# Optimization experiments

Measured on AMD Instinct MI355X. Metric: run time of the kernel, lower is better.

## Reference

```python
import jax, jax.numpy as jnp
import numpy as np

DIM = 768
NUM_HEADS = 12
HEAD_DIM = DIM // NUM_HEADS
SCALE = HEAD_DIM ** -0.5


def setup_inputs() -> dict:
    key = jax.random.key(0)
    ks = jax.random.split(key, 5)
    b, n = 8, 1024
    x = jax.random.normal(ks[0], (b, n, DIM), dtype=jnp.float32)
    # qkv Linear weight: torch stores (out, in) = (3*DIM, DIM)
    w_qkv = jax.random.normal(ks[1], (3 * DIM, DIM), dtype=jnp.float32) * (DIM ** -0.5)
    q_bias = jax.random.normal(ks[2], (DIM,), dtype=jnp.float32) * 0.02
    v_bias = jax.random.normal(ks[3], (DIM,), dtype=jnp.float32) * 0.02
    w_proj = jax.random.normal(ks[4], (DIM, DIM), dtype=jnp.float32) * (DIM ** -0.5)
    b_proj = jnp.zeros((DIM,), dtype=jnp.float32)
    return {"x": x, "w_qkv": w_qkv, "q_bias": q_bias, "v_bias": v_bias,
            "w_proj": w_proj, "b_proj": b_proj}


def reference(x, w_qkv, q_bias, v_bias, w_proj, b_proj):
    b, n, _ = x.shape
    # qkv bias: [q_bias, zeros, v_bias]
    qkv_bias = jnp.concatenate([q_bias, jnp.zeros_like(v_bias), v_bias])
    qkv = x @ w_qkv.T + qkv_bias                      # (b, n, 3*DIM)
    qkv = qkv.reshape(b, n, 3, NUM_HEADS, HEAD_DIM)
    qkv = jnp.transpose(qkv, (2, 0, 3, 1, 4))          # (3, b, h, n, d)
    q, k, v = qkv[0], qkv[1], qkv[2]
    q = q * SCALE
    attn = jnp.einsum('bhqd,bhkd->bhqk', q, k)         # (b, h, n, n)
    attn = jax.nn.softmax(attn, axis=-1)
    out = jnp.einsum('bhqk,bhkd->bhqd', attn, v)       # (b, h, n, d)
    out = jnp.transpose(out, (0, 2, 1, 3)).reshape(b, n, NUM_HEADS * HEAD_DIM)
    return out @ w_proj.T + b_proj
```

## Files before the change

### kernel.cpp

```cpp
#include <hip/hip_runtime.h>
#include <math.h>

#define BATCH 8
#define SEQ   1024
#define DIM   768
#define NH    12
#define HD    64
#define MROWS 8192
#define NQKV  2304
#define KDIM  768
#define QSCALE 0.18033688011112042f

typedef unsigned short u16;
typedef unsigned int   u32;
typedef __attribute__((ext_vector_type(8))) short bf16x8;
typedef __attribute__((ext_vector_type(4))) float f32x4;
typedef __attribute__((ext_vector_type(16))) float f32x16;

__device__ __forceinline__ u16 f2bf(float f){
  u32 u = __builtin_bit_cast(u32, f);
  u += 0x7FFFu + ((u >> 16) & 1u);
  return (u16)(u >> 16);
}

__device__ __forceinline__ void gload16(const void* g, void* l){
  __builtin_amdgcn_global_load_lds((const __attribute__((address_space(1))) u32*)g,
                                   (__attribute__((address_space(3))) u32*)l, 16, 0, 0);
}

__device__ __forceinline__ f32x16 zero16(){
  return (f32x16){0.f,0.f,0.f,0.f,0.f,0.f,0.f,0.f,0.f,0.f,0.f,0.f,0.f,0.f,0.f,0.f};
}

__global__ __launch_bounds__(256) void convert_bf16(
    const float* __restrict__ x, const float* __restrict__ wq,
    const float* __restrict__ wp, u16* __restrict__ xb,
    u16* __restrict__ wqb, u16* __restrict__ wpb){
  const long n1 = (long)MROWS*DIM/8, n2 = (long)NQKV*DIM/8, n3 = (long)DIM*DIM/8;
  long i = (long)blockIdx.x*blockDim.x + threadIdx.x;
  const float* s; u16* d;
  if (i < n1)            { s = x  + i*8;        d = xb  + i*8; }
  else if (i < n1+n2)    { long j=i-n1;    s = wq + j*8; d = wqb + j*8; }
  else if (i < n1+n2+n3) { long j=i-n1-n2; s = wp + j*8; d = wpb + j*8; }
  else return;
  float4 a = ((const float4*)s)[0];
  float4 b = ((const float4*)s)[1];
  union { u16 h[8]; uint4 v; } o;
  o.h[0]=f2bf(a.x); o.h[1]=f2bf(a.y); o.h[2]=f2bf(a.z); o.h[3]=f2bf(a.w);
  o.h[4]=f2bf(b.x); o.h[5]=f2bf(b.y); o.h[6]=f2bf(b.z); o.h[7]=f2bf(b.w);
  *((uint4*)d) = o.v;
}

__global__ __launch_bounds__(512, 4) void qkv_gemm(
    const u16* __restrict__ xb, const u16* __restrict__ wb,
    const float* __restrict__ qbias, const float* __restrict__ vbias,
    u16* __restrict__ qo, u16* __restrict__ ko, u16* __restrict__ vto){
  __shared__ u16 As[16384];
  __shared__ u16 Bs[16384];
  const int tid = threadIdx.x;
  const int wid = tid >> 6, lane = tid & 63;
  const int lr = lane & 15, lg = lane >> 4;
  const int wm = wid >> 2, wn = wid & 3;
  const int swz = (blockIdx.x & 7) * 144 + (blockIdx.x >> 3);
  const int bm = swz / 18, bn = swz % 18;
  const int mbase = bm * 128, nbase = bn * 128;
  const int sr8 = tid >> 3;
  const int sc8 = ((tid & 7) ^ (sr8 & 7)) * 8;
  const u16* aS = xb + (size_t)(mbase + sr8) * KDIM + sc8;
  const u16* bS = wb + (size_t)(nbase + sr8) * KDIM + sc8;
  u16* aD = As + tid * 8;
  u16* bD = Bs + tid * 8;

#define STAGEQ(buf, k0) do {                                                  \
    gload16(aS + (k0),            aD + (buf)*8192);                           \
    gload16(aS + (k0) + 64*KDIM,  aD + (buf)*8192 + 4096);                    \
    gload16(bS + (k0),            bD + (buf)*8192);                           \
    gload16(bS + (k0) + 64*KDIM,  bD + (buf)*8192 + 4096);                    \
  } while(0)

  f32x4 acc[4][2];
  #pragma unroll
  for (int a=0;a<4;++a)
    #pragma unroll
    for (int b=0;b<2;++b) acc[a][b] = (f32x4){0.f,0.f,0.f,0.f};

  STAGEQ(0, 0);
  __syncthreads();

  for (int kt = 0; kt < 12; ++kt){
    const int cur = kt & 1;
    if (kt < 11) STAGEQ(cur ^ 1, (kt+1)*64);
    const u16* Ac = As + cur*8192;
    const u16* Bc = Bs + cur*8192;
    bf16x8 af[2][4], bfv[2][2];
    #pragma unroll
    for (int kk = 0; kk < 2; ++kk){
      const int ch = (((kk*4 + lg)) ^ (lr & 7)) * 8;
      #pragma unroll
      for (int f = 0; f < 4; ++f)
        af[kk][f]  = *(const bf16x8*)(Ac + (wm*64 + f*16 + lr)*64 + ch);
      #pragma unroll
      for (int g = 0; g < 2; ++g)
        bfv[kk][g] = *(const bf16x8*)(Bc + (wn*32 + g*16 + lr)*64 + ch);
    }
    #pragma unroll
    for (int fm = 0; fm < 4; ++fm)
      #pragma unroll
      for (int fn = 0; fn < 2; ++fn){
        acc[fm][fn] = __builtin_amdgcn_mfma_f32_16x16x32_bf16(af[0][fm], bfv[0][fn], acc[fm][fn], 0,0,0);
        acc[fm][fn] = __builtin_amdgcn_mfma_f32_16x16x32_bf16(af[1][fm], bfv[1][fn], acc[fm][fn], 0,0,0);
      }
    __syncthreads();
  }
#undef STAGEQ

  const int which = bn / 6;
  const int bb = mbase >> 10, nn0 = mbase & 1023;
  if (which == 2){
    const int vcol0 = nbase - 1536;
    float bv[2];
    #pragma unroll
    for (int fn = 0; fn < 2; ++fn) bv[fn] = vbias[vcol0 + wn*32 + fn*16 + lr];
    u16* Ls = As;
    #pragma unroll
    for (int h = 0; h < 2; ++h){
      __syncthreads();
      if (wm == h){
        #pragma unroll
        for (int fn = 0; fn < 2; ++fn){
          const int n = wn*32 + fn*16 + lr;
          #pragma unroll
          for (int fm = 0; fm < 4; ++fm)
            #pragma unroll
            for (int r = 0; r < 4; ++r){
              const int mloc = fm*16 + lg*4 + r;
              Ls[n*64 + (((mloc>>3) ^ (n&7))*8) + (mloc&7)] = f2bf(acc[fm][fn][r] + bv[fn]);
            }
        }
      }
      __syncthreads();
      const int n = tid >> 2, q4 = tid & 3;
      const int col = vcol0 + n;
      u16* drow = vto + ((size_t)((bb*NH + (col>>6))*HD + (col&63)))*SEQ + nn0 + h*64;
      #pragma unroll
      for (int j2 = 0; j2 < 2; ++j2){
        const int j = q4*2 + j2;
        *(uint4*)(drow + j*8) = *(const uint4*)(Ls + n*64 + ((j ^ (n&7))*8));
      }
    }
  } else {
    const int mrow0 = mbase + wm*64;
    const int ncol0 = nbase - which*768 + wn*32;
    #pragma unroll
    for (int fn = 0; fn < 2; ++fn){
      const int col = ncol0 + fn*16 + lr;
      const int hh = col >> 6, dd = col & 63;
      const float bias = (which == 0) ? qbias[col] : 0.f;
      #pragma unroll
      for (int fm = 0; fm < 4; ++fm){
        #pragma unroll
        for (int r = 0; r < 4; ++r){
          const int m = mrow0 + fm*16 + lg*4 + r;
          const int head = (m >> 10)*NH + hh;
          const float v = acc[fm][fn][r] + bias;
          if (which == 0) qo[((size_t)head*SEQ + (m & 1023))*HD + dd] = f2bf(v * QSCALE);
          else            ko[((size_t)head*SEQ + (m & 1023))*HD + dd] = f2bf(v);
        }
      }
    }
  }
}

__global__ __launch_bounds__(256, 3) void attn_kernel(
    const u16* __restrict__ qg, const u16* __restrict__ kg,
    const u16* __restrict__ vtg, u16* __restrict__ og){
  __shared__ u16 Ks[3*4096];
  __shared__ u16 VTs[3*4096];
  const int tid  = threadIdx.x;
  const int wid  = tid >> 6, lane = tid & 63;
  const int l31  = lane & 31, hi = lane >> 5, l7 = lane & 7;
  const int bid  = blockIdx.x;
  const int swz  = (bid & 7) * 96 + (bid >> 3);
  const int head = swz >> 3;
  const int qbase = (swz & 7) * 128;
  const u16* Q  = qg  + (size_t)head * SEQ * HD;
  const u16* K  = kg  + (size_t)head * SEQ * HD;
  const u16* VT = vtg + (size_t)head * HD * SEQ;

  const int qrow = qbase + wid*32 + l31;
  bf16x8 qf[4];
  #pragma unroll
  for (int dc = 0; dc < 4; ++dc)
    qf[dc] = *(const bf16x8*)(Q + (size_t)qrow*HD + dc*16 + hi*8);

  f32x16 oacc[2];
  oacc[0] = zero16(); oacc[1] = zero16();
  float lrow = 0.f;

  bf16x8 vfr[8];
  bf16x8 pa[4];

  const int srow   = lane >> 3;
  const int schunk = ((lane & 7) ^ srow) * 8;

#define STAGE(bufi, kv0) do {                                                 \
    const u16* ksrc = K + (size_t)((kv0) + wid*16 + srow)*HD + schunk;        \
    gload16(ksrc,         &Ks[(bufi)*4096 + wid*1024]);                       \
    gload16(ksrc + 8*HD,  &Ks[(bufi)*4096 + wid*1024 + 512]);                 \
    const u16* vsrc = VT + (size_t)(wid*16 + srow)*SEQ + (kv0) + schunk;      \
    gload16(vsrc,         &VTs[(bufi)*4096 + wid*1024]);                      \
    gload16(vsrc + 8*SEQ, &VTs[(bufi)*4096 + wid*1024 + 512]);                \
  } while(0)

  STAGE(0, 0);
  STAGE(1, 64);

  #pragma unroll
  for (int t = 0; t < 16; ++t){
    const int cur = t % 3;
    if (t < 15) asm volatile("s_waitcnt vmcnt(4) lgkmcnt(0)" ::: "memory");
    else        asm volatile("s_waitcnt vmcnt(0) lgkmcnt(0)" ::: "memory");
    __builtin_amdgcn_s_barrier();
    if (t < 14) STAGE((t+2)%3, (t+2)*64);

    const u16* Kc  = &Ks[cur*4096];
    const u16* VTc = &VTs[cur*4096];

    f32x16 sv[2];
    __builtin_amdgcn_s_setprio(1);
    #pragma unroll
    for (int b = 0; b < 2; ++b){
      sv[b] = zero16();
      #pragma unroll
      for (int dc = 0; dc < 4; ++dc){
        bf16x8 kf = *(const bf16x8*)(&Kc[(b*32 + l31)*64 + (((dc*2 + hi) ^ l7) * 8)]);
        sv[b] = __builtin_amdgcn_mfma_f32_32x32x16_bf16(kf, qf[dc], sv[b], 0,0,0);
      }
    }
    if (t > 0){
      #pragma unroll
      for (int kc = 0; kc < 4; ++kc)
        #pragma unroll
        for (int db = 0; db < 2; ++db)
          oacc[db] = __builtin_amdgcn_mfma_f32_32x32x16_bf16(pa[kc], vfr[kc*2+db], oacc[db], 0,0,0);
    }
    __builtin_amdgcn_s_setprio(0);

    #pragma unroll
    for (int kc = 0; kc < 4; ++kc)
      #pragma unroll
      for (int db = 0; db < 2; ++db)
        vfr[kc*2+db] = *(const bf16x8*)(&VTc[(db*32 + l31)*64 + (((kc*2 + hi) ^ l7) * 8)]);

    float tsum[16];
    #pragma unroll
    for (int i = 0; i < 16; ++i){
      float p0 = __builtin_amdgcn_exp2f(sv[0][i]);
      float p1 = __builtin_amdgcn_exp2f(sv[1][i]);
      sv[0][i] = p0; sv[1][i] = p1;
      tsum[i] = p0 + p1;
    }
    #pragma unroll
    for (int st = 8; st > 0; st >>= 1)
      #pragma unroll
      for (int i = 0; i < st; ++i) tsum[i] += tsum[i + st];
    const float ssum = tsum[0];
    lrow += ssum + __shfl_xor(ssum, 32);

    #pragma unroll
    for (int b = 0; b < 2; ++b){
      u32 x0,x1,x2,x3,y0,y1,y2,y3;
      asm("v_cvt_pk_bf16_f32 %0, %1, %2" : "=v"(x0) : "v"(sv[b][0]),  "v"(sv[b][1]));
      asm("v_cvt_pk_bf16_f32 %0, %1, %2" : "=v"(y0) : "v"(sv[b][4]),  "v"(sv[b][5]));
      asm("v_cvt_pk_bf16_f32 %0, %1, %2" : "=v"(x1) : "v"(sv[b][2]),  "v"(sv[b][3]));
      asm("v_cvt_pk_bf16_f32 %0, %1, %2" : "=v"(y1) : "v"(sv[b][6]),  "v"(sv[b][7]));
      asm("v_permlane32_swap_b32 %0, %1" : "+v"(x0), "+v"(y0));
      asm("v_permlane32_swap_b32 %0, %1" : "+v"(x1), "+v"(y1));
      asm("v_cvt_pk_bf16_f32 %0, %1, %2" : "=v"(x2) : "v"(sv[b][8]),  "v"(sv[b][9]));
      asm("v_cvt_pk_bf16_f32 %0, %1, %2" : "=v"(y2) : "v"(sv[b][12]), "v"(sv[b][13]));
      asm("v_cvt_pk_bf16_f32 %0, %1, %2" : "=v"(x3) : "v"(sv[b][10]), "v"(sv[b][11]));
      asm("v_cvt_pk_bf16_f32 %0, %1, %2" : "=v"(y3) : "v"(sv[b][14]), "v"(sv[b][15]));
      asm("v_permlane32_swap_b32 %0, %1" : "+v"(x2), "+v"(y2));
      asm("v_permlane32_swap_b32 %0, %1" : "+v"(x3), "+v"(y3));
      union { u32 w[4]; bf16x8 f; } fa, fb;
      fa.w[0]=x0; fa.w[1]=x1; fa.w[2]=y0; fa.w[3]=y1;
      fb.w[0]=x2; fb.w[1]=x3; fb.w[2]=y2; fb.w[3]=y3;
      pa[b*2]   = fa.f;
      pa[b*2+1] = fb.f;
    }
  }
#undef STAGE

  __builtin_amdgcn_s_setprio(1);
  #pragma unroll
  for (int kc = 0; kc < 4; ++kc)
    #pragma unroll
    for (int db = 0; db < 2; ++db)
      oacc[db] = __builtin_amdgcn_mfma_f32_32x32x16_bf16(pa[kc], vfr[kc*2+db], oacc[db], 0,0,0);
  __builtin_amdgcn_s_setprio(0);

  const float inv = 1.f / lrow;
  const int bb = head / NH, hh = head % NH;
  #pragma unroll
  for (int r = 0; r < 16; ++r){
    const int q = (r&3) + 8*(r>>2) + 4*hi;
    const float s = __shfl(inv, q);
    const int n = qbase + wid*32 + q;
    u16* orow = og + (size_t)(bb*SEQ + n)*DIM + hh*HD;
    orow[l31]      = f2bf(oacc[0][r] * s);
    orow[32 + l31] = f2bf(oacc[1][r] * s);
  }
}

__global__ __launch_bounds__(256) void proj_gemm(
    const u16* __restrict__ ab, const u16* __restrict__ wb,
    const float* __restrict__ bias, float* __restrict__ out){
  __shared__ u16 As2[2*4096];
  __shared__ u16 Bs2[2*8192];
  const int tid = threadIdx.x;
  const int wid = tid >> 6, lane = tid & 63;
  const int lr = lane & 15, lg = lane >> 4;
  const int wm = wid >> 1, wn = wid & 1;
  const int swz = (blockIdx.x & 7) * 96 + (blockIdx.x >> 3);
  const int bm = swz / 6, bn = swz % 6;
  const int mbase = bm * 64, nbase = bn * 128;
  const int sr8 = tid >> 3;
  const int sc8 = ((tid & 7) ^ (sr8 & 7)) * 8;
  const u16* aS = ab + (size_t)(mbase + sr8) * KDIM + sc8;
  const u16* bS = wb + (size_t)(nbase + sr8) * KDIM + sc8;
  u16* aD = As2 + tid * 8;
  u16* bD = Bs2 + tid * 8;

#define STAGEP(buf, k0) do {                                                  \
    gload16(aS + (k0),            aD + (buf)*4096);                           \
    gload16(aS + (k0) + 32*KDIM,  aD + (buf)*4096 + 2048);                    \
    _Pragma("unroll")                                                         \
    for (int i = 0; i < 4; ++i)                                               \
      gload16(bS + (k0) + (size_t)i*32*KDIM, bD + (buf)*8192 + i*2048);       \
  } while(0)

  f32x4 acc[2][4];
  #pragma unroll
  for (int a=0;a<2;++a)
    #pragma unroll
    for (int b=0;b<4;++b) acc[a][b] = (f32x4){0.f,0.f,0.f,0.f};

  STAGEP(0, 0);
  __syncthreads();

  for (int kt = 0; kt < 12; ++kt){
    const int cur = kt & 1;
    if (kt < 11) STAGEP(cur ^ 1, (kt+1)*64);
    const u16* Ac = As2 + cur*4096;
    const u16* Bc = Bs2 + cur*8192;
    bf16x8 af[2][2], bfv[2][4];
    #pragma unroll
    for (int kk = 0; kk < 2; ++kk){
      const int ch = (((kk*4 + lg)) ^ (lr & 7)) * 8;
      #pragma unroll
      for (int f = 0; f < 2; ++f)
        af[kk][f]  = *(const bf16x8*)(Ac + (wm*32 + f*16 + lr)*64 + ch);
      #pragma unroll
      for (int g = 0; g < 4; ++g)
        bfv[kk][g] = *(const bf16x8*)(Bc + (wn*64 + g*16 + lr)*64 + ch);
    }
    #pragma unroll
    for (int fm = 0; fm < 2; ++fm)
      #pragma unroll
      for (int fn = 0; fn < 4; ++fn){
        acc[fm][fn] = __builtin_amdgcn_mfma_f32_16x16x32_bf16(af[0][fm], bfv[0][fn], acc[fm][fn], 0,0,0);
        acc[fm][fn] = __builtin_amdgcn_mfma_f32_16x16x32_bf16(af[1][fm], bfv[1][fn], acc[fm][fn], 0,0,0);
      }
    __syncthreads();
  }
#undef STAGEP

  const int mrow0 = mbase + wm*32;
  const int ncol0 = nbase + wn*64;
  #pragma unroll
  for (int fn = 0; fn < 4; ++fn){
    const int col = ncol0 + fn*16 + lr;
    const float bv = bias[col];
    #pragma unroll
    for (int fm = 0; fm < 2; ++fm){
      #pragma unroll
      for (int r = 0; r < 4; ++r){
        const int m = mrow0 + fm*16 + lg*4 + r;
        out[(size_t)m*DIM + col] = acc[fm][fn][r] + bv;
      }
    }
  }
}

extern "C" void kernel_launch(void* const* d_in, const int* in_sizes, int n_in,
                              void* d_out, int out_size, void* d_ws, size_t ws_size,
                              hipStream_t stream) {
  const float* x      = (const float*)d_in[0];
  const float* w_qkv  = (const float*)d_in[1];
  const float* q_bias = (const float*)d_in[2];
  const float* v_bias = (const float*)d_in[3];
  const float* w_proj = (const float*)d_in[4];
  const float* b_proj = (const float*)d_in[5];
  float* out = (float*)d_out;
  char* ws = (char*)d_ws;
  u16* xb  = (u16*)(ws);
  u16* wqb = (u16*)(ws + 12582912);
  u16* wpb = (u16*)(ws + 16121856);
  u16* qbf = (u16*)(ws + 17301504);
  u16* kbf = (u16*)(ws + 29884416);
  u16* vtb = (u16*)(ws + 42467328);
  u16* abf = (u16*)(ws + 55050240);

  convert_bf16<<<4224, 256, 0, stream>>>(x, w_qkv, w_proj, xb, wqb, wpb);
  qkv_gemm   <<<64*18, 512, 0, stream>>>(xb, wqb, q_bias, v_bias, qbf, kbf, vtb);
  attn_kernel<<<96*8,  256, 0, stream>>>(qbf, kbf, vtb, abf);
  proj_gemm  <<<128*6, 256, 0, stream>>>(abf, wpb, b_proj, out);
}
```

Measured before the change: 106.6 us.

## Use triple-buffered K=32 LDS pipeline with single barrier in QKV GEMM

Reworks the QKV GEMM main loop from double-buffered 64-wide K tiles to triple-buffered 32-wide K tiles. It waits with an explicit vmcnt so two loads stay in flight, and uses one barrier per step instead of two syncs. LDS use drops, which is meant to let the raised launch-bounds occupancy (6 blocks) fit. The cost is more loop iterations with fewer MFMAs each, plus a new swizzle and hand-placed waitcnt logic that could be fragile.

```diff
diff --git a/kernel.cpp b/kernel.cpp
--- a/kernel.cpp
+++ b/kernel.cpp
@@ -51,12 +51,12 @@
   *((uint4*)d) = o.v;
 }
 
-__global__ __launch_bounds__(512, 4) void qkv_gemm(
+__global__ __launch_bounds__(512, 6) void qkv_gemm(
     const u16* __restrict__ xb, const u16* __restrict__ wb,
     const float* __restrict__ qbias, const float* __restrict__ vbias,
     u16* __restrict__ qo, u16* __restrict__ ko, u16* __restrict__ vto){
-  __shared__ u16 As[16384];
-  __shared__ u16 Bs[16384];
+  __shared__ u16 As[3*4096];
+  __shared__ u16 Bs[3*4096];
   const int tid = threadIdx.x;
   const int wid = tid >> 6, lane = tid & 63;
   const int lr = lane & 15, lg = lane >> 4;
@@ -64,18 +64,17 @@
   const int swz = (blockIdx.x & 7) * 144 + (blockIdx.x >> 3);
   const int bm = swz / 18, bn = swz % 18;
   const int mbase = bm * 128, nbase = bn * 128;
-  const int sr8 = tid >> 3;
-  const int sc8 = ((tid & 7) ^ (sr8 & 7)) * 8;
-  const u16* aS = xb + (size_t)(mbase + sr8) * KDIM + sc8;
-  const u16* bS = wb + (size_t)(nbase + sr8) * KDIM + sc8;
+  const int tr = tid >> 2;
+  const int lc = ((tid & 3) ^ ((tr ^ (tr >> 2)) & 3));
+  const u16* aS = xb + (size_t)(mbase + tr) * KDIM + lc*8;
+  const u16* bS = wb + (size_t)(nbase + tr) * KDIM + lc*8;
   u16* aD = As + tid * 8;
   u16* bD = Bs + tid * 8;
+  const int rch = ((lg ^ lr ^ (lr >> 2)) & 3) * 8;
 
 #define STAGEQ(buf, k0) do {                                                  \
-    gload16(aS + (k0),            aD + (buf)*8192);                           \
-    gload16(aS + (k0) + 64*KDIM,  aD + (buf)*8192 + 4096);                    \
-    gload16(bS + (k0),            bD + (buf)*8192);                           \
-    gload16(bS + (k0) + 64*KDIM,  bD + (buf)*8192 + 4096);                    \
+    gload16(aS + (k0), aD + (buf)*4096);                                      \
+    gload16(bS + (k0), bD + (buf)*4096);                                      \
   } while(0)
 
   f32x4 acc[4][2];
@@ -85,32 +84,29 @@
     for (int b=0;b<2;++b) acc[a][b] = (f32x4){0.f,0.f,0.f,0.f};
 
   STAGEQ(0, 0);
-  __syncthreads();
-
-  for (int kt = 0; kt < 12; ++kt){
-    const int cur = kt & 1;
-    if (kt < 11) STAGEQ(cur ^ 1, (kt+1)*64);
-    const u16* Ac = As + cur*8192;
-    const u16* Bc = Bs + cur*8192;
-    bf16x8 af[2][4], bfv[2][2];
-    #pragma unroll
-    for (int kk = 0; kk < 2; ++kk){
-      const int ch = (((kk*4 + lg)) ^ (lr & 7)) * 8;
-      #pragma unroll
-      for (int f = 0; f < 4; ++f)
-        af[kk][f]  = *(const bf16x8*)(Ac + (wm*64 + f*16 + lr)*64 + ch);
-      #pragma unroll
-      for (int g = 0; g < 2; ++g)
-        bfv[kk][g] = *(const bf16x8*)(Bc + (wn*32 + g*16 + lr)*64 + ch);
-    }
+  STAGEQ(1, 32);
+
+  #pragma unroll
+  for (int t = 0; t < 24; ++t){
+    const int cur = t % 3;
+    if (t < 23) asm volatile("s_waitcnt vmcnt(2) lgkmcnt(0)" ::: "memory");
+    else        asm volatile("s_waitcnt vmcnt(0) lgkmcnt(0)" ::: "memory");
+    __builtin_amdgcn_s_barrier();
+    if (t < 22) STAGEQ((t+2)%3, (t+2)*32);
+    const u16* Ac = As + cur*4096;
+    const u16* Bc = Bs + cur*4096;
+    bf16x8 af[4], bfv[2];
+    #pragma unroll
+    for (int f = 0; f < 4; ++f)
+      af[f]  = *(const bf16x8*)(Ac + (wm*64 + f*16 + lr)*32 + rch);
+    #pragma unroll
+    for (int g = 0; g < 2; ++g)
+      bfv[g] = *(const bf16x8*)(Bc + (wn*32 + g*16 + lr)*32 + rch);
     #pragma unroll
     for (int fm = 0; fm < 4; ++fm)
       #pragma unroll
-      for (int fn = 0; fn < 2; ++fn){
-        acc[fm][fn] = __builtin_amdgcn_mfma_f32_16x16x32_bf16(af[0][fm], bfv[0][fn], acc[fm][fn], 0,0,0);
-        acc[fm][fn] = __builtin_amdgcn_mfma_f32_16x16x32_bf16(af[1][fm], bfv[1][fn], acc[fm][fn], 0,0,0);
-      }
-    __syncthreads();
+      for (int fn = 0; fn < 2; ++fn)
+        acc[fm][fn] = __builtin_amdgcn_mfma_f32_16x16x32_bf16(af[fm], bfv[fn], acc[fm][fn], 0,0,0);
   }
 #undef STAGEQ
 
```

Result: no change. 105.6 us (-0.9%).
